# Kernel optimization log

Hardware: AMD Instinct MI355X
Metric: run time of the kernel (lower is better)

Reference implementation:

```python
import jax, jax.numpy as jnp
import numpy as np

HID = 16  # module-level output_size constant
D = 64    # input_dim
K = 32    # number of classes / outer nets
B = 8192  # batch


def setup_inputs() -> dict:
    key = jax.random.key(0)
    ks = jax.random.split(key, 9)
    s = 0.1
    return {
        "x": jax.random.normal(ks[0], (B, D), dtype=jnp.float32),
        # inner nets: one tiny 1->16->1 MLP per (k, i)
        "iw1": jax.random.normal(ks[1], (K, D, HID), dtype=jnp.float32) * s,  # Linear(1,16) weight
        "ib1": jax.random.normal(ks[2], (K, D, HID), dtype=jnp.float32) * s,  # Linear(1,16) bias
        "iw2": jax.random.normal(ks[3], (K, D, HID), dtype=jnp.float32) * s,  # Linear(16,1) weight
        "ib2": jax.random.normal(ks[4], (K, D), dtype=jnp.float32) * s,       # Linear(16,1) bias
        # outer nets: one 1->16->1 MLP per k
        "ow1": jax.random.normal(ks[5], (K, HID), dtype=jnp.float32) * s,
        "ob1": jax.random.normal(ks[6], (K, HID), dtype=jnp.float32) * s,
        "ow2": jax.random.normal(ks[7], (K, HID), dtype=jnp.float32) * s,
        "ob2": jax.random.normal(ks[8], (K,), dtype=jnp.float32) * s,
    }


def reference(x, iw1, ib1, iw2, ib2, ow1, ob1, ow2, ob2):
    # Inner nets, all K*D at once. Linear(1,HID) on scalar xi is an outer product.
    # h: [B, K, D, HID]
    h = jax.nn.relu(x[:, None, :, None] * iw1[None] + ib1[None])
    # Linear(HID,1): contract HID -> yi: [B, K, D]
    yi = jnp.einsum('bkdh,kdh->bkd', h, iw2) + ib2[None]
    # sum over input features i -> [B, K]
    sk = yi.sum(axis=2)
    # Outer nets: scalar -> HID -> scalar per k
    g = jax.nn.relu(sk[:, :, None] * ow1[None] + ob1[None])  # [B, K, HID]
    out = jnp.einsum('bkh,kh->bk', g, ow2) + ob2[None]       # [B, K]
    return out
```

## Files before the change

### kernel.cpp

```cpp
#include <hip/hip_runtime.h>
#include <hip/hip_bf16.h>

#define HID 16
#define DIN 64
#define NK  32
#define NB  8192

typedef float v2f __attribute__((ext_vector_type(2)));
typedef float v4f __attribute__((ext_vector_type(4)));

struct W {
    v2f w1[8], b1[8], w2[8];
};

__device__ __forceinline__ float relu_dot(const W& w, float xd) {
    const v2f xx = {xd, xd};
    v2f acc0 = {0.f, 0.f}, acc1 = {0.f, 0.f};
    #pragma unroll
    for (int hp = 0; hp < 8; hp += 2) {
        v2f t0 = __builtin_elementwise_fma(xx, w.w1[hp],     w.b1[hp]);
        v2f t1 = __builtin_elementwise_fma(xx, w.w1[hp + 1], w.b1[hp + 1]);
        t0 = __builtin_elementwise_max(t0, (v2f){0.f, 0.f});
        t1 = __builtin_elementwise_max(t1, (v2f){0.f, 0.f});
        acc0 = __builtin_elementwise_fma(t0, w.w2[hp],     acc0);
        acc1 = __builtin_elementwise_fma(t1, w.w2[hp + 1], acc1);
    }
    const v2f a = acc0 + acc1;
    return a.x + a.y;
}

__global__ __launch_bounds__(256, 4) void kan_kernel(
    const float* __restrict__ x,
    const float* __restrict__ iw1, const float* __restrict__ ib1,
    const float* __restrict__ iw2, const float* __restrict__ ib2,
    const float* __restrict__ ow1, const float* __restrict__ ob1,
    const float* __restrict__ ow2, const float* __restrict__ ob2,
    float* __restrict__ out)
{
    __shared__ float lds[4][DIN * 17];

    const int t    = threadIdx.x;
    const int lane = t & 63;
    const int wid  = t >> 6;
    const int k    = blockIdx.x & (NK - 1);
    const int base = ((blockIdx.x >> 5) * 4 + wid) * 64;

    W w;
    {
        const v4f* p1 = (const v4f*)(iw1 + (k * DIN + lane) * HID);
        const v4f* p2 = (const v4f*)(ib1 + (k * DIN + lane) * HID);
        const v4f* p3 = (const v4f*)(iw2 + (k * DIN + lane) * HID);
        #pragma unroll
        for (int q = 0; q < 4; ++q) {
            ((v4f*)w.w1)[q] = p1[q];
            ((v4f*)w.b1)[q] = p2[q];
            ((v4f*)w.w2)[q] = p3[q];
        }
    }

    float ck = ib2[k * DIN + lane];
    #pragma unroll
    for (int m = 32; m; m >>= 1) ck += __shfl_xor(ck, m, 64);

    float* __restrict__ myLds = lds[wid];
    const float* __restrict__ xp = x + base * DIN + lane;

    const int jj = lane & 15;
    const int p  = lane >> 4;

    float rsum[4];

    #pragma unroll
    for (int pass = 0; pass < 4; ++pass) {
        const float* __restrict__ xq = xp + pass * 16 * DIN;
        #pragma unroll
        for (int j = 0; j < 16; ++j) {
            myLds[lane * 17 + j] = relu_dot(w, xq[j * DIN]);
        }
        __builtin_amdgcn_sched_barrier(0);
        float s = 0.f;
        #pragma unroll
        for (int i = 0; i < 16; ++i) {
            s += myLds[(p * 16 + i) * 17 + jj];
        }
        __builtin_amdgcn_sched_barrier(0);
        s += __shfl_xor(s, 16, 64);
        s += __shfl_xor(s, 32, 64);
        rsum[pass] = s + ck;
    }

    const float sk = (lane & 32) ? ((lane & 16) ? rsum[3] : rsum[2])
                                 : ((lane & 16) ? rsum[1] : rsum[0]);

    float o = ob2[k];
    #pragma unroll
    for (int h = 0; h < HID; ++h) {
        const float g = fmaxf(fmaf(sk, ow1[k * HID + h], ob1[k * HID + h]), 0.f);
        o = fmaf(g, ow2[k * HID + h], o);
    }

    out[(base + lane) * NK + k] = o;
}

extern "C" void kernel_launch(void* const* d_in, const int* in_sizes, int n_in,
                              void* d_out, int out_size, void* d_ws, size_t ws_size,
                              hipStream_t stream) {
    const float* x   = (const float*)d_in[0];
    const float* iw1 = (const float*)d_in[1];
    const float* ib1 = (const float*)d_in[2];
    const float* iw2 = (const float*)d_in[3];
    const float* ib2 = (const float*)d_in[4];
    const float* ow1 = (const float*)d_in[5];
    const float* ob1 = (const float*)d_in[6];
    const float* ow2 = (const float*)d_in[7];
    const float* ob2 = (const float*)d_in[8];
    float* out = (float*)d_out;

    const int grid = (NB / 256) * NK;
    kan_kernel<<<grid, 256, 0, stream>>>(x, iw1, ib1, iw2, ib2,
                                         ow1, ob1, ow2, ob2, out);
}
```

Baseline: 26.49 us.

## Rewrite inner ReLU MLP as abs-based piecewise-linear form and prefetch x

Uses relu(z) = (z+|z|)/2 to fold the linear part of each inner 1->16->1 MLP into a per-lane affine term A*x+B, leaving 16 abs-plus-FMA terms of the form u*|x+c| instead of fma+max+fma per hidden unit. The ib2 bias reduction is folded into B. It also software-prefetches the next 16 x values into registers while the current pass is evaluated, and drops the sched_barriers. The trade-off is extra register pressure from xr/xn, a division per hidden unit at setup, and possible floating-point differences from the reformulation (division by w1, a threshold for near-zero weights).

```diff
diff --git a/kernel.cpp b/kernel.cpp
--- a/kernel.cpp
+++ b/kernel.cpp
@@ -9,24 +9,23 @@
 typedef float v2f __attribute__((ext_vector_type(2)));
 typedef float v4f __attribute__((ext_vector_type(4)));
 
-struct W {
-    v2f w1[8], b1[8], w2[8];
+struct PW {
+    float A, B;
+    float u[HID];
+    v2f   c[HID / 2];
 };
 
-__device__ __forceinline__ float relu_dot(const W& w, float xd) {
+__device__ __forceinline__ float pl_eval(const PW& w, float xd) {
+    float a0 = fmaf(w.A, xd, w.B);
+    float a1 = 0.f;
     const v2f xx = {xd, xd};
-    v2f acc0 = {0.f, 0.f}, acc1 = {0.f, 0.f};
     #pragma unroll
-    for (int hp = 0; hp < 8; hp += 2) {
-        v2f t0 = __builtin_elementwise_fma(xx, w.w1[hp],     w.b1[hp]);
-        v2f t1 = __builtin_elementwise_fma(xx, w.w1[hp + 1], w.b1[hp + 1]);
-        t0 = __builtin_elementwise_max(t0, (v2f){0.f, 0.f});
-        t1 = __builtin_elementwise_max(t1, (v2f){0.f, 0.f});
-        acc0 = __builtin_elementwise_fma(t0, w.w2[hp],     acc0);
-        acc1 = __builtin_elementwise_fma(t1, w.w2[hp + 1], acc1);
+    for (int hp = 0; hp < HID / 2; ++hp) {
+        const v2f t = xx + w.c[hp];
+        a0 = fmaf(fabsf(t.x), w.u[2 * hp],     a0);
+        a1 = fmaf(fabsf(t.y), w.u[2 * hp + 1], a1);
     }
-    const v2f a = acc0 + acc1;
-    return a.x + a.y;
+    return a0 + a1;
 }
 
 __global__ __launch_bounds__(256, 4) void kan_kernel(
@@ -45,22 +44,32 @@
     const int k    = blockIdx.x & (NK - 1);
     const int base = ((blockIdx.x >> 5) * 4 + wid) * 64;
 
-    W w;
+    PW w;
     {
+        v4f w1v[4], b1v[4], w2v[4];
         const v4f* p1 = (const v4f*)(iw1 + (k * DIN + lane) * HID);
         const v4f* p2 = (const v4f*)(ib1 + (k * DIN + lane) * HID);
         const v4f* p3 = (const v4f*)(iw2 + (k * DIN + lane) * HID);
         #pragma unroll
-        for (int q = 0; q < 4; ++q) {
-            ((v4f*)w.w1)[q] = p1[q];
-            ((v4f*)w.b1)[q] = p2[q];
-            ((v4f*)w.w2)[q] = p3[q];
+        for (int q = 0; q < 4; ++q) { w1v[q] = p1[q]; b1v[q] = p2[q]; w2v[q] = p3[q]; }
+
+        float A = 0.f;
+        float B = ib2[k * DIN + lane];
+        #pragma unroll
+        for (int h = 0; h < HID; ++h) {
+            const float w1 = w1v[h >> 2][h & 3];
+            const float b1 = b1v[h >> 2][h & 3];
+            const float w2 = w2v[h >> 2][h & 3];
+            A = fmaf(0.5f * w2, w1, A);
+            B = fmaf(0.5f * w2, b1, B);
+            const float aw = fabsf(w1);
+            const bool ok  = aw > 1e-20f;
+            w.c[h >> 1][h & 1] = ok ? (b1 / w1) : 0.f;
+            w.u[h]             = ok ? (0.5f * w2 * aw) : 0.f;
+            if (!ok) B += 0.5f * w2 * fabsf(b1);
         }
+        w.A = A; w.B = B;
     }
-
-    float ck = ib2[k * DIN + lane];
-    #pragma unroll
-    for (int m = 32; m; m >>= 1) ck += __shfl_xor(ck, m, 64);
 
     float* __restrict__ myLds = lds[wid];
     const float* __restrict__ xp = x + base * DIN + lane;
@@ -68,25 +77,32 @@
     const int jj = lane & 15;
     const int p  = lane >> 4;
 
-    float rsum[4];
+    float xr[16], xn[16], rsum[4];
+
+    #pragma unroll
+    for (int j = 0; j < 16; ++j) xr[j] = xp[j * DIN];
 
     #pragma unroll
     for (int pass = 0; pass < 4; ++pass) {
-        const float* __restrict__ xq = xp + pass * 16 * DIN;
+        if (pass < 3) {
+            const float* __restrict__ xq = xp + (pass + 1) * 16 * DIN;
+            #pragma unroll
+            for (int j = 0; j < 16; ++j) xn[j] = xq[j * DIN];
+        }
         #pragma unroll
         for (int j = 0; j < 16; ++j) {
-            myLds[lane * 17 + j] = relu_dot(w, xq[j * DIN]);
+            myLds[lane * 17 + j] = pl_eval(w, xr[j]);
         }
-        __builtin_amdgcn_sched_barrier(0);
         float s = 0.f;
         #pragma unroll
         for (int i = 0; i < 16; ++i) {
             s += myLds[(p * 16 + i) * 17 + jj];
         }
-        __builtin_amdgcn_sched_barrier(0);
         s += __shfl_xor(s, 16, 64);
         s += __shfl_xor(s, 32, 64);
-        rsum[pass] = s + ck;
+        rsum[pass] = s;
+        #pragma unroll
+        for (int j = 0; j < 16; ++j) xr[j] = xn[j];
     }
 
     const float sk = (lane & 32) ? ((lane & 16) ? rsum[3] : rsum[2])
```

After: 27.36 us. 1.03x slower.
